# Kernel optimization log

Hardware: AMD Instinct MI355X
Metric: run time of the kernel (lower is better)

The kernel has to match this reference:

```python
import jax, jax.numpy as jnp
import numpy as np

N = 512    # hidden states
M = 4096   # emission symbols
B = 64     # batch
TMAX = 512 # max sequence length


def setup_inputs() -> dict:
    key = jax.random.key(0)
    k1, k2, k3, k4, k5 = jax.random.split(key, 5)
    x = jax.random.randint(k1, (B, TMAX), 0, M)                       # observations
    T = jax.random.randint(k2, (B,), 1, TMAX + 1)                     # lengths in [1, TMAX]
    emission_logits = jax.random.normal(k3, (N, M), dtype=jnp.float32)
    transition_logits = jax.random.normal(k4, (N, N), dtype=jnp.float32)
    prior_logits = jax.random.normal(k5, (N,), dtype=jnp.float32)
    return {
        "x": x,
        "T": T,
        "emission_logits": emission_logits,
        "transition_logits": transition_logits,
        "prior_logits": prior_logits,
    }


def reference(x, T, emission_logits, transition_logits, prior_logits):
    # Normalize once (the torch code recomputes log_softmax every step; same math).
    log_em = jax.nn.log_softmax(emission_logits, axis=1)      # (N, M), row-stochastic
    log_tr = jax.nn.log_softmax(transition_logits, axis=0)    # (N, N), column-stochastic: tr[j,k] = p(j|k)
    log_pri = jax.nn.log_softmax(prior_logits, axis=0)        # (N,)

    obs = log_em.T[x]                                         # (B, TMAX, N): log p(x_t | state)

    log_alpha0 = obs[:, 0, :] + log_pri                       # (B, N)

    def step(log_alpha, obs_t):
        # new[b, j] = obs_t[b, j] + logsumexp_k( log_tr[j, k] + log_alpha[b, k] )
        new = obs_t + jax.nn.logsumexp(log_alpha[:, None, :] + log_tr[None, :, :], axis=2)
        return new, new

    _, rest = jax.lax.scan(step, log_alpha0, jnp.swapaxes(obs[:, 1:, :], 0, 1))
    log_alpha = jnp.concatenate([log_alpha0[:, None, :], jnp.swapaxes(rest, 0, 1)], axis=1)  # (B, TMAX, N)

    log_sums = jax.nn.logsumexp(log_alpha, axis=2)            # (B, TMAX)
    log_probs = jnp.take_along_axis(log_sums, (T - 1)[:, None], axis=1)  # (B, 1)
    return log_probs
```

## Files before the change

### kernel.cpp

```cpp
#include <hip/hip_runtime.h>
#include <math.h>

#define HN 512
#define HM 4096
#define HB 64
#define HT 512

#if __has_builtin(__builtin_amdgcn_udot8)
  #define ENC_BIASED 0
  __device__ __forceinline__ int dot8q(unsigned int a, unsigned int b, int c){
    return (int)__builtin_amdgcn_udot8(a, b, (unsigned int)c, false);
  }
#elif __has_builtin(__builtin_amdgcn_sdot8)
  #define ENC_BIASED 1
  __device__ __forceinline__ int dot8q(unsigned int a, unsigned int b, int c){
    return __builtin_amdgcn_sdot8((int)a, (int)b, c, false);
  }
#else
  #define ENC_BIASED 0
  __device__ __forceinline__ int dot4u8f(unsigned int a, unsigned int b, int c){
#if __has_builtin(__builtin_amdgcn_sdot4)
    return __builtin_amdgcn_sdot4((int)a, (int)b, c, false);
#else
    c += (int)(a & 0xffu)       * (int)(b & 0xffu);
    c += (int)((a>>8) & 0xffu)  * (int)((b>>8) & 0xffu);
    c += (int)((a>>16) & 0xffu) * (int)((b>>16) & 0xffu);
    c += (int)(a>>24)           * (int)(b>>24);
    return c;
#endif
  }
  __device__ __forceinline__ int dot8q(unsigned int a, unsigned int b, int c){
    unsigned int al = a & 0x0F0F0F0Fu, ah = (a>>4) & 0x0F0F0F0Fu;
    unsigned int bl = b & 0x0F0F0F0Fu, bh = (b>>4) & 0x0F0F0F0Fu;
    c = dot4u8f(al, bl, c);
    return dot4u8f(ah, bh, c);
  }
#endif

__device__ __forceinline__ float rcpf(float x){
#if __has_builtin(__builtin_amdgcn_rcpf)
  return __builtin_amdgcn_rcpf(x);
#else
  return 1.0f / x;
#endif
}

__device__ __forceinline__ float wsum(float v){
  #pragma unroll
  for(int o=32;o>0;o>>=1) v += __shfl_xor(v,o,64);
  return v;
}
__device__ __forceinline__ float wmax(float v){
  #pragma unroll
  for(int o=32;o>0;o>>=1) v = fmaxf(v,__shfl_xor(v,o,64));
  return v;
}

#if __has_builtin(__builtin_amdgcn_update_dpp) && __has_builtin(__builtin_amdgcn_readlane)
#define HAVE_DPP 1
#define DPPF(v, ctrl, rmask) \
  __int_as_float(__builtin_amdgcn_update_dpp(0, __float_as_int(v), (ctrl), (rmask), 0xf, true))
__device__ __forceinline__ float wsum_nn(float v){
  v += DPPF(v, 0x111, 0xf);
  v += DPPF(v, 0x112, 0xf);
  v += DPPF(v, 0x114, 0xf);
  v += DPPF(v, 0x118, 0xf);
  v += DPPF(v, 0x142, 0xa);
  v += DPPF(v, 0x143, 0xc);
  return __int_as_float(__builtin_amdgcn_readlane(__float_as_int(v), 63));
}
__device__ __forceinline__ float wmax_nn(float v){
  v = fmaxf(v, DPPF(v, 0x111, 0xf));
  v = fmaxf(v, DPPF(v, 0x112, 0xf));
  v = fmaxf(v, DPPF(v, 0x114, 0xf));
  v = fmaxf(v, DPPF(v, 0x118, 0xf));
  v = fmaxf(v, DPPF(v, 0x142, 0xa));
  v = fmaxf(v, DPPF(v, 0x143, 0xc));
  return __int_as_float(__builtin_amdgcn_readlane(__float_as_int(v), 63));
}
__device__ __forceinline__ int xor1_i(int v){
  return __builtin_amdgcn_update_dpp(0, v, 0x0B1, 0xf, 0xf, true);
}
#else
#define HAVE_DPP 0
__device__ __forceinline__ float wsum_nn(float v){ return wsum(v); }
__device__ __forceinline__ float wmax_nn(float v){ return wmax(v); }
__device__ __forceinline__ int xor1_i(int v){ return __shfl_xor(v, 1, 64); }
#endif

__device__ __forceinline__ float blockSum512(float v, float* red, float* bc){
  v = wsum(v);
  if((threadIdx.x & 63)==0) red[threadIdx.x>>6] = v;
  __syncthreads();
  if(threadIdx.x < 64){
    float s = (threadIdx.x<8)? red[threadIdx.x] : 0.0f;
    #pragma unroll
    for(int o=4;o>0;o>>=1) s += __shfl_xor(s,o,64);
    if(threadIdx.x==0) *bc = s;
  }
  __syncthreads();
  return *bc;
}
__device__ __forceinline__ float blockMax512(float v, float* red, float* bc){
  v = wmax(v);
  if((threadIdx.x & 63)==0) red[threadIdx.x>>6] = v;
  __syncthreads();
  if(threadIdx.x < 64){
    float s = (threadIdx.x<8)? red[threadIdx.x] : -INFINITY;
    #pragma unroll
    for(int o=4;o>0;o>>=1) s = fmaxf(s, __shfl_xor(s,o,64));
    if(threadIdx.x==0) *bc = s;
  }
  __syncthreads();
  return *bc;
}

__device__ __forceinline__ unsigned short f2bf(float f){
  unsigned int u = __float_as_uint(f);
  unsigned int r = (u + 0x7fffu + ((u>>16)&1u)) >> 16;
  return (unsigned short)r;
}
__device__ __forceinline__ float bf2f(unsigned int w){ return __uint_as_float(w<<16); }


__global__ __launch_bounds__(512) void k_em_lse(const float* __restrict__ em, float* __restrict__ em_lse){
  __shared__ float red[8]; __shared__ float bc;
  int r = blockIdx.x;
  const float* row = em + (size_t)r*HM;
  float mx = -INFINITY;
  for(int i=threadIdx.x;i<HM;i+=512) mx = fmaxf(mx, row[i]);
  mx = blockMax512(mx, red, &bc);
  float s = 0.f;
  for(int i=threadIdx.x;i<HM;i+=512) s += expf(row[i]-mx);
  s = blockSum512(s, red, &bc);
  if(threadIdx.x==0) em_lse[r] = mx + logf(s);
}

__global__ __launch_bounds__(512) void k_pri(const float* __restrict__ pri, float* __restrict__ P, float* __restrict__ pric){
  __shared__ float red[8]; __shared__ float bc;
  int j = threadIdx.x;
  float v = pri[j];
  float mx = blockMax512(v, red, &bc);
  float w = expf(v-mx);
  float s = blockSum512(w, red, &bc);
  P[j] = w;
  if(j==0) *pric = -logf(s);
}

__global__ __launch_bounds__(256) void k_em_tab(const float* __restrict__ em, const float* __restrict__ em_lse,
                                                unsigned short* __restrict__ emT){
  __shared__ unsigned short tile[64][66];
  __shared__ float lsl[64];
  int m0 = blockIdx.x*64, j0 = blockIdx.y*64;
  int tx = threadIdx.x & 63, ty = threadIdx.x >> 6;
  if(threadIdx.x < 64) lsl[threadIdx.x] = em_lse[j0 + threadIdx.x];
  __syncthreads();
  #pragma unroll
  for(int r=0;r<16;r++){
    int jl = ty*16 + r;
    float v = em[(size_t)(j0+jl)*HM + m0 + tx];
    tile[jl][tx] = f2bf(expf(v - lsl[jl]));
  }
  __syncthreads();
  #pragma unroll
  for(int r=0;r<16;r++){
    int ml = ty*16 + r;
    emT[(size_t)(m0+ml)*HN + j0 + tx] = tile[tx][ml];
  }
}

__global__ __launch_bounds__(512) void k_trcol(const float* __restrict__ tr,
                                               float* __restrict__ cmax, float* __restrict__ csum){
  __shared__ float red[8]; __shared__ float bc;
  int k = blockIdx.x, j = threadIdx.x;
  float v = tr[(size_t)j*HN + k];
  float mx = blockMax512(v, red, &bc);
  float s  = blockSum512(expf(v-mx), red, &bc);
  if(j==0){ cmax[k] = mx; csum[k] = s; }
}

__global__ __launch_bounds__(512) void k_trrow(const float* __restrict__ tr,
                                               const float* __restrict__ cmax, const float* __restrict__ csum,
                                               unsigned char* __restrict__ TQ4,
                                               float* __restrict__ rscale, float* __restrict__ rbar,
                                               unsigned short* __restrict__ tsumq){
  __shared__ float red[8]; __shared__ float bc;
  int j = blockIdx.x, k = threadIdx.x;
  float v = expf(tr[(size_t)j*HN + k] - cmax[k]) / csum[k];
  float rm = blockMax512(v, red, &bc);
  int q = __float2int_rn(v * (15.0f/rm));
  float rs = blockSum512(v, red, &bc);
  float qs = blockSum512((float)q, red, &bc);
  float wq = wsum((float)q);
  int qn = __shfl_down(q, 1, 64);
  if((k & 1)==0){
#if ENC_BIASED
    unsigned char by = (unsigned char)(((q-8)&0xF) | (((qn-8)&0xF)<<4));
#else
    unsigned char by = (unsigned char)((q&0xF) | ((qn&0xF)<<4));
#endif
    TQ4[(size_t)j*256 + ((k>>5)<<4) + ((k&31)>>1)] = by;
  }
  if((k&63)==0) tsumq[j*8 + (k>>6)] = (unsigned short)(int)wq;
  if(k==0){
    rscale[j] = rm * (1.0f/15.0f);
    rbar[j]   = rs - (rm * (1.0f/15.0f)) * qs;
  }
}

__global__ __launch_bounds__(512, 1)
void k_fwd(const int* __restrict__ x, const int* __restrict__ Tl,
           const unsigned short* __restrict__ emTu,
           const float* __restrict__ P, const float* __restrict__ pric,
           const float* __restrict__ rscaleG, const float* __restrict__ rbarG,
           const unsigned short* __restrict__ tsumqG,
           const uint4* __restrict__ TQd4,
           float* __restrict__ out){
  extern __shared__ char smem[];
  uint4*         apl4  = (uint4*)smem;
  unsigned char* aplB  = (unsigned char*)smem;
  float*         sigS  = (float*)(smem + 512);
  float*         sumS  = (float*)(smem + 576);
  float*         aqS   = (float*)(smem + 640);
  float*         rawS  = (float*)(smem + 704);
  int*           xls   = (int*)(smem + 768);
  float*         rscL  = (float*)(smem + 2816);
  float*         rbarL = (float*)(smem + 4864);
  unsigned short* tsumL= (unsigned short*)(smem + 6912);

  const int t = threadIdx.x, b = blockIdx.x, w = t>>6, L = t&63;
  const int j = t;

  unsigned int trq[64];
  #pragma unroll
  for(int q=0;q<16;q++) ((uint4*)trq)[q] = TQd4[j*16 + q];
  #pragma unroll
  for(int r=0;r<64;r++) asm volatile("" : "+v"(trq[r]));

  xls[t]   = x[b*HT + t];
  rscL[t]  = rscaleG[t];
  rbarL[t] = rbarG[t];
  for(int d=t; d<2048; d+=512) ((unsigned int*)tsumL)[d] = ((const unsigned int*)tsumqG)[d];
  int Tb = Tl[b];
  __syncthreads();

  int m = xls[0];
  float e0 = bf2f((unsigned)emTu[(size_t)m*HN + j]);
  float nvr = e0 * P[j];
  {
    float s = wsum_nn(nvr);
    if(L==0) rawS[w] = s;
  }
  __syncthreads();
  float4 q0 = ((float4*)rawS)[0], q1 = ((float4*)rawS)[1];
  float S0 = ((q0.x+q0.y)+(q0.z+q0.w))+((q1.x+q1.y)+(q1.z+q1.w));
  float c_acc = pric[0] + __logf(S0);
  float nvd = nvr * rcpf(S0);
  {
    float Mw = fmaxf(wmax_nn(nvd), 1e-30f);
    float sig = Mw * (1.0f/15.0f);
    int aq = __float2int_rn(nvd * (15.0f * rcpf(Mw)));
    float Sw = wsum_nn(nvd);
#if ENC_BIASED
    float AqSw = wsum_nn((float)aq);
#endif
    int aqn = xor1_i(aq);
    if((j&1)==0){
#if ENC_BIASED
      aplB[256 + (j>>1)] = (unsigned char)(((aq-8)&0xF) | (((aqn-8)&0xF)<<4));
#else
      aplB[256 + (j>>1)] = (unsigned char)((aq&0xF) | ((aqn&0xF)<<4));
#endif
    }
    if(L==0){
      sigS[8+w] = sig; sumS[8+w] = Sw;
#if ENC_BIASED
      aqS[8+w] = AqSw;
#endif
    }
  }
  int mn = xls[(Tb>1)?1:0];
  float eC = bf2f((unsigned)emTu[(size_t)mn*HN + j]);
  const float rsc = rscL[j], rbr = rbarL[j];

  for(int tt=1; tt<Tb; tt++){
    __syncthreads();
    const int rb = (tt & 1), wb = rb ^ 1;

    int acc[8];
    #pragma unroll
    for(int i=0;i<8;i++) acc[i] = 0;
    const uint4* aplR = apl4 + 16*rb;
    #pragma unroll
    for(int c=0;c<16;c++){
      uint4 A = aplR[c];
      int wi = c>>1;
      acc[wi] = dot8q(trq[4*c+0], A.x, acc[wi]);
      acc[wi] = dot8q(trq[4*c+1], A.y, acc[wi]);
      acc[wi] = dot8q(trq[4*c+2], A.z, acc[wi]);
      acc[wi] = dot8q(trq[4*c+3], A.w, acc[wi]);
    }

    float4 g0 = ((float4*)(sumS + 8*rb))[0], g1 = ((float4*)(sumS + 8*rb))[1];
    float Sp = ((g0.x+g0.y)+(g0.z+g0.w))+((g1.x+g1.y)+(g1.z+g1.w));
    if(tt > 1) c_acc += __logf(Sp);
    float d_inv = rcpf(Sp);
    float abar  = Sp * (1.0f/512.0f);
    float4 s0 = ((float4*)(sigS + 8*rb))[0], s1 = ((float4*)(sigS + 8*rb))[1];
    float sg[8] = {s0.x,s0.y,s0.z,s0.w,s1.x,s1.y,s1.z,s1.w};

    float Af = 0.f;
#if ENC_BIASED
    {
      float4 a0 = ((float4*)(aqS + 8*rb))[0], a1 = ((float4*)(aqS + 8*rb))[1];
      float av[8] = {a0.x,a0.y,a0.z,a0.w,a1.x,a1.y,a1.z,a1.w};
      uint4 tq = ((const uint4*)tsumL)[j];
      int ts[8] = {(int)(tq.x&0xffff),(int)(tq.x>>16),(int)(tq.y&0xffff),(int)(tq.y>>16),
                   (int)(tq.z&0xffff),(int)(tq.z>>16),(int)(tq.w&0xffff),(int)(tq.w>>16)};
      #pragma unroll
      for(int i=0;i<8;i++)
        Af += sg[i] * (float)(acc[i] + 8*(ts[i] + (int)av[i]) - 4096);
    }
#else
    #pragma unroll
    for(int i=0;i<8;i++) Af += sg[i] * (float)acc[i];
#endif
    float D = rsc * Af + abar * rbr;
    nvd = fmaxf(D * eC * d_inv, 0.0f);

    int tn = (tt+1 < HT)? tt+1 : HT-1;
    mn = xls[tn];
    float eN = bf2f((unsigned)emTu[(size_t)mn*HN + j]);

    float Mw = fmaxf(wmax_nn(nvd), 1e-30f);
    float sig = Mw * (1.0f/15.0f);
    int aq = __float2int_rn(nvd * (15.0f * rcpf(Mw)));
    float Sw = wsum_nn(nvd);
#if ENC_BIASED
    float AqSw = wsum_nn((float)aq);
#endif
    int aqn = xor1_i(aq);
    if((j&1)==0){
#if ENC_BIASED
      aplB[256*wb + (j>>1)] = (unsigned char)(((aq-8)&0xF) | (((aqn-8)&0xF)<<4));
#else
      aplB[256*wb + (j>>1)] = (unsigned char)((aq&0xF) | ((aqn&0xF)<<4));
#endif
    }
    if(L==0){
      sigS[8*wb+w] = sig; sumS[8*wb+w] = Sw;
#if ENC_BIASED
      aqS[8*wb+w] = AqSw;
#endif
    }
    eC = eN;
  }

  __syncthreads();
  {
    const int fb = (Tb & 1);
    float4 g0 = ((float4*)(sumS + 8*fb))[0], g1 = ((float4*)(sumS + 8*fb))[1];
    float Sf = ((g0.x+g0.y)+(g0.z+g0.w))+((g1.x+g1.y)+(g1.z+g1.w));
    if(t==0) out[b] = c_acc + __logf(Sf);
  }
}

extern "C" void kernel_launch(void* const* d_in, const int* in_sizes, int n_in,
                              void* d_out, int out_size, void* d_ws, size_t ws_size,
                              hipStream_t stream){
  const int*   x   = (const int*)d_in[0];
  const int*   T   = (const int*)d_in[1];
  const float* em  = (const float*)d_in[2];
  const float* tr  = (const float*)d_in[3];
  const float* pri = (const float*)d_in[4];
  float* out = (float*)d_out;

  char* ws = (char*)d_ws;
  float* em_lse = (float*)ws;
  float* P      = (float*)(ws + 2048);
  float* pric   = (float*)(ws + 4096);
  float* cmax   = (float*)(ws + 8192);
  float* csum   = (float*)(ws + 10240);
  float* rscale = (float*)(ws + 12288);
  float* rbar   = (float*)(ws + 14336);
  unsigned short* tsumq = (unsigned short*)(ws + 16384);
  unsigned short* emT = (unsigned short*)(ws + 24576);
  unsigned char*  TQ4 = (unsigned char*)(ws + 24576 + (size_t)HM*HN*2);

  k_em_lse<<<HN, 512, 0, stream>>>(em, em_lse);
  k_pri   <<<1,  512, 0, stream>>>(pri, P, pric);
  k_trcol <<<HN, 512, 0, stream>>>(tr, cmax, csum);
  k_trrow <<<HN, 512, 0, stream>>>(tr, cmax, csum, TQ4, rscale, rbar, tsumq);
  k_em_tab<<<dim3(HM/64, HN/64), 256, 0, stream>>>(em, em_lse, emT);

  const int lds_bytes = 15104;
  (void)hipFuncSetAttribute((const void*)k_fwd, hipFuncAttributeMaxDynamicSharedMemorySize, lds_bytes);
  k_fwd<<<HB, 512, lds_bytes, stream>>>(x, T, emT, P, pric, rscale, rbar, tsumq,
                                        (const uint4*)TQ4, out);
}
```

Before: 502.9 us.

## Park quantized transition rows in AGPRs and broadcast alpha via readlane

Moves the 64 packed 4-bit transition words per thread from VGPRs into accumulation registers (AGPRs) using inline accvgpr writes and reads, and requests two waves per EU. It also replaces the 16 vector LDS loads of the quantized alpha with one 32-bit LDS load per lane, followed by scalar readlane broadcasts feeding the dot8 instructions. The aim is to cut VGPR pressure so more waves fit, and to reduce LDS traffic in the serial time loop. In exchange each step now runs 64 extra accvgpr reads and 64 readlanes, which may lengthen the per-step critical path.

```diff
diff --git a/kernel.cpp b/kernel.cpp
--- a/kernel.cpp
+++ b/kernel.cpp
@@ -208,7 +208,7 @@
   }
 }
 
-__global__ __launch_bounds__(512, 1)
+__global__ __launch_bounds__(512) __attribute__((amdgpu_waves_per_eu(2, 2)))
 void k_fwd(const int* __restrict__ x, const int* __restrict__ Tl,
            const unsigned short* __restrict__ emTu,
            const float* __restrict__ P, const float* __restrict__ pric,
@@ -231,11 +231,29 @@
   const int t = threadIdx.x, b = blockIdx.x, w = t>>6, L = t&63;
   const int j = t;
 
-  unsigned int trq[64];
-  #pragma unroll
-  for(int q=0;q<16;q++) ((uint4*)trq)[q] = TQd4[j*16 + q];
-  #pragma unroll
-  for(int r=0;r<64;r++) asm volatile("" : "+v"(trq[r]));
+  const uint4* trp = TQd4 + (size_t)j*16;
+  unsigned int ag0, ag1, ag2, ag3, ag4, ag5, ag6, ag7;
+  unsigned int ag8, ag9, ag10, ag11, ag12, ag13, ag14, ag15;
+  unsigned int ag16, ag17, ag18, ag19, ag20, ag21, ag22, ag23;
+  unsigned int ag24, ag25, ag26, ag27, ag28, ag29, ag30, ag31;
+  unsigned int ag32, ag33, ag34, ag35, ag36, ag37, ag38, ag39;
+  unsigned int ag40, ag41, ag42, ag43, ag44, ag45, ag46, ag47;
+  unsigned int ag48, ag49, ag50, ag51, ag52, ag53, ag54, ag55;
+  unsigned int ag56, ag57, ag58, ag59, ag60, ag61, ag62, ag63;
+#define STG4(q, A0, A1, A2, A3) { uint4 tv = trp[q]; \
+  asm volatile("v_accvgpr_write_b32 %0, %1" : "=a"(A0) : "v"(tv.x)); \
+  asm volatile("v_accvgpr_write_b32 %0, %1" : "=a"(A1) : "v"(tv.y)); \
+  asm volatile("v_accvgpr_write_b32 %0, %1" : "=a"(A2) : "v"(tv.z)); \
+  asm volatile("v_accvgpr_write_b32 %0, %1" : "=a"(A3) : "v"(tv.w)); }
+  STG4(0,  ag0,  ag1,  ag2,  ag3)   STG4(1,  ag4,  ag5,  ag6,  ag7)
+  STG4(2,  ag8,  ag9,  ag10, ag11)  STG4(3,  ag12, ag13, ag14, ag15)
+  STG4(4,  ag16, ag17, ag18, ag19)  STG4(5,  ag20, ag21, ag22, ag23)
+  STG4(6,  ag24, ag25, ag26, ag27)  STG4(7,  ag28, ag29, ag30, ag31)
+  STG4(8,  ag32, ag33, ag34, ag35)  STG4(9,  ag36, ag37, ag38, ag39)
+  STG4(10, ag40, ag41, ag42, ag43)  STG4(11, ag44, ag45, ag46, ag47)
+  STG4(12, ag48, ag49, ag50, ag51)  STG4(13, ag52, ag53, ag54, ag55)
+  STG4(14, ag56, ag57, ag58, ag59)  STG4(15, ag60, ag61, ag62, ag63)
+#undef STG4
 
   xls[t]   = x[b*HT + t];
   rscL[t]  = rscaleG[t];
@@ -287,19 +305,31 @@
     __syncthreads();
     const int rb = (tt & 1), wb = rb ^ 1;
 
+    unsigned int aw = *(const unsigned int*)(aplB + 256*rb + (L<<2));
     int acc[8];
     #pragma unroll
     for(int i=0;i<8;i++) acc[i] = 0;
-    const uint4* aplR = apl4 + 16*rb;
-    #pragma unroll
-    for(int c=0;c<16;c++){
-      uint4 A = aplR[c];
-      int wi = c>>1;
-      acc[wi] = dot8q(trq[4*c+0], A.x, acc[wi]);
-      acc[wi] = dot8q(trq[4*c+1], A.y, acc[wi]);
-      acc[wi] = dot8q(trq[4*c+2], A.z, acc[wi]);
-      acc[wi] = dot8q(trq[4*c+3], A.w, acc[wi]);
-    }
+#define DOT1(d, Areg) { unsigned int r_; \
+    asm volatile("v_accvgpr_read_b32 %0, %1" : "=v"(r_) : "a"(Areg)); \
+    unsigned int ad_ = (unsigned int)__builtin_amdgcn_readlane((int)aw, (d)); \
+    acc[(d)>>3] = dot8q(ad_, r_, acc[(d)>>3]); }
+    DOT1(0,  ag0)  DOT1(1,  ag1)  DOT1(2,  ag2)  DOT1(3,  ag3)
+    DOT1(4,  ag4)  DOT1(5,  ag5)  DOT1(6,  ag6)  DOT1(7,  ag7)
+    DOT1(8,  ag8)  DOT1(9,  ag9)  DOT1(10, ag10) DOT1(11, ag11)
+    DOT1(12, ag12) DOT1(13, ag13) DOT1(14, ag14) DOT1(15, ag15)
+    DOT1(16, ag16) DOT1(17, ag17) DOT1(18, ag18) DOT1(19, ag19)
+    DOT1(20, ag20) DOT1(21, ag21) DOT1(22, ag22) DOT1(23, ag23)
+    DOT1(24, ag24) DOT1(25, ag25) DOT1(26, ag26) DOT1(27, ag27)
+    DOT1(28, ag28) DOT1(29, ag29) DOT1(30, ag30) DOT1(31, ag31)
+    DOT1(32, ag32) DOT1(33, ag33) DOT1(34, ag34) DOT1(35, ag35)
+    DOT1(36, ag36) DOT1(37, ag37) DOT1(38, ag38) DOT1(39, ag39)
+    DOT1(40, ag40) DOT1(41, ag41) DOT1(42, ag42) DOT1(43, ag43)
+    DOT1(44, ag44) DOT1(45, ag45) DOT1(46, ag46) DOT1(47, ag47)
+    DOT1(48, ag48) DOT1(49, ag49) DOT1(50, ag50) DOT1(51, ag51)
+    DOT1(52, ag52) DOT1(53, ag53) DOT1(54, ag54) DOT1(55, ag55)
+    DOT1(56, ag56) DOT1(57, ag57) DOT1(58, ag58) DOT1(59, ag59)
+    DOT1(60, ag60) DOT1(61, ag61) DOT1(62, ag62) DOT1(63, ag63)
+#undef DOT1
 
     float4 g0 = ((float4*)(sumS + 8*rb))[0], g1 = ((float4*)(sumS + 8*rb))[1];
     float Sp = ((g0.x+g0.y)+(g0.z+g0.w))+((g1.x+g1.y)+(g1.z+g1.w));
```

Result: slower. 737.4 us (+46.6%).
